# Optimization experiments

Hardware: AMD Instinct MI355X
Metric: run time of the kernel (lower is better)

Reference implementation:

```python
import jax, jax.numpy as jnp
import numpy as np
from jax import lax

N, CIN, COUT = 4, 3, 16
D = H = W = 64
K, S, PAD, OUT_PAD = 3, 2, 1, 1


def setup_inputs() -> dict:
    key = jax.random.key(0)
    k1, k2, k3, k4 = jax.random.split(key, 4)
    x = jax.random.normal(k1, (N, CIN, D, H, W), dtype=jnp.float32)
    # torch ConvTranspose3d weight layout: [Cin, Cout, kD, kH, kW]
    w = jax.random.normal(k2, (CIN, COUT, K, K, K), dtype=jnp.float32) * 0.1
    b = jax.random.normal(k3, (COUT,), dtype=jnp.float32) * 0.1
    subtract = jax.random.normal(k4, (COUT,), dtype=jnp.float32) * 0.1
    return {"x": x, "w": w, "b": b, "subtract": subtract}


def reference(x, w, b, subtract):
    # ConvTranspose3d(k=3, s=2, p=1, output_padding=1) as a dilated conv:
    # flip kernel spatially, swap in/out channel axes, lhs_dilation = stride,
    # padding low = k-1-p = 1, padding high = k-1-p+output_padding = 2.
    w_conv = jnp.flip(jnp.transpose(w, (1, 0, 2, 3, 4)), axis=(2, 3, 4))  # [Cout,Cin,k,k,k]
    y = lax.conv_general_dilated(
        x, w_conv,
        window_strides=(1, 1, 1),
        padding=[(1, 2), (1, 2), (1, 2)],
        lhs_dilation=(S, S, S),
        dimension_numbers=("NCDHW", "OIDHW", "NCDHW"),
    )  # [N, 16, 2D, 2H, 2W]
    y = y + b[None, :, None, None, None]
    # MaxPool3d(kernel=2, stride=2, pad=0)
    y = lax.reduce_window(
        y, -jnp.inf, lax.max,
        window_dimensions=(1, 1, 2, 2, 2),
        window_strides=(1, 1, 2, 2, 2),
        padding="VALID",
    )  # [N, 16, D, H, W]
    s = jax.nn.softmax(y, axis=1)                       # channel softmax
    z = s - subtract[None, :, None, None, None]          # per-channel subtract
    sw = z * jax.nn.sigmoid(z)                           # swish
    return jnp.max(sw, axis=1)                           # max over channels -> [N, D, H, W]
```

## Files before the change

kernel.cpp:

```cpp
#include <hip/hip_runtime.h>
#include <math.h>

#define CIN 3
#define COUT 16
#define DHW 64


typedef float f8 __attribute__((ext_vector_type(8)));
typedef float f2 __attribute__((ext_vector_type(2)));

struct WBuf { f8 a, b, c; f2 d2; float dl; };

template <int G>
static __device__ __forceinline__ void wload(WBuf& b, const char* wbase) {
    constexpr int J = G / 3, C = G % 3;
    constexpr int BOFF = (C * COUT + J) * 27 * 4;
    asm volatile(
        "s_load_dwordx8 %0, %5, %6\n\t"
        "s_load_dwordx8 %1, %5, %7\n\t"
        "s_load_dwordx8 %2, %5, %8\n\t"
        "s_load_dwordx2 %3, %5, %9\n\t"
        "s_load_dword   %4, %5, %10"
        : "=&s"(b.a), "=&s"(b.b), "=&s"(b.c), "=&s"(b.d2), "=&s"(b.dl)
        : "s"(wbase), "i"(BOFF), "i"(BOFF + 32), "i"(BOFF + 64),
          "i"(BOFF + 96), "i"(BOFF + 104));
}

static __device__ __forceinline__ void wwait(WBuf& b) {
    asm volatile("s_waitcnt lgkmcnt(0)"
                 : "+s"(b.a), "+s"(b.b), "+s"(b.c), "+s"(b.d2), "+s"(b.dl));
}

static __device__ __forceinline__ float welem(const WBuf& w, int k) {
    return k < 8 ? w.a[k] : k < 16 ? w.b[k - 8] : k < 24 ? w.c[k - 16]
                 : k < 26 ? w.d2[k - 24] : w.dl;
}

template <int C>
static __device__ __forceinline__ void fma_group(
    const WBuf& wb, const float (&xr)[CIN][3][2][3], float (&acc)[8][4]) {
#pragma unroll
    for (int kd = 0; kd < 3; ++kd) {
        const int pd  = (kd == 1) ? 0 : 1;
        const int dlt = (kd == 0) ? 1 : 0;
#pragma unroll
        for (int kh = 0; kh < 3; ++kh) {
            const int ph = (kh == 1) ? 0 : 1;
            const int hh = (kh == 0) ? 1 : 0;
#pragma unroll
            for (int kw = 0; kw < 3; ++kw) {
                const int pw = (kw == 1) ? 0 : 1;
                const int ww = (kw == 0) ? 1 : 0;
                const float wt = welem(wb, kd * 9 + kh * 3 + kw);
                const int q = (pd * 2 + ph) * 2 + pw;
#pragma unroll
                for (int dout = 0; dout < 2; ++dout)
#pragma unroll
                    for (int vx = 0; vx < 2; ++vx) {
                        const float xv = xr[C][dout + dlt][hh][ww + vx];
                        const int v = dout * 2 + vx;
                        if (C == 0 && kd < 2 && kh < 2 && kw < 2)
                            acc[q][v] = wt * xv;
                        else
                            acc[q][v] = fmaf(wt, xv, acc[q][v]);
                    }
            }
        }
    }
}

static __device__ __forceinline__ void pool_close(const float (&acc)[8][4],
                                                  float (&pc)[4]) {
#pragma unroll
    for (int v = 0; v < 4; ++v) {
        const float m01 = fmaxf(acc[0][v], acc[1][v]);
        const float m23 = fmaxf(acc[2][v], acc[3][v]);
        const float m45 = fmaxf(acc[4][v], acc[5][v]);
        const float m67 = fmaxf(acc[6][v], acc[7][v]);
        pc[v] = fmaxf(fmaxf(m01, m23), fmaxf(m45, m67));
    }
}

template <int G>
struct Pipe {
    static __device__ __forceinline__ void run(
        WBuf& A, WBuf& B, const char* wbase, const float (&xr)[CIN][3][2][3],
        float (&acc)[8][4], float (&pooled)[4][4]) {
        constexpr int J = G / 3, C = G % 3;
        WBuf& CUR = (G & 1) ? B : A;
        WBuf& NXT = (G & 1) ? A : B;
        wwait(CUR);
        __builtin_amdgcn_sched_barrier(0);
        if constexpr (G + 1 < 4 * CIN) wload<G + 1>(NXT, wbase);
        fma_group<C>(CUR, xr, acc);
        if constexpr (C == 2) pool_close(acc, pooled[J]);
        Pipe<G + 1>::run(A, B, wbase, xr, acc, pooled);
    }
};
template <>
struct Pipe<4 * CIN> {
    static __device__ __forceinline__ void run(
        WBuf&, WBuf&, const char*, const float (&)[CIN][3][2][3],
        float (&)[8][4], float (&)[4][4]) {}
};

__global__ __launch_bounds__(256) void fused_convt_pool_softmax_swish_max(
    const float* __restrict__ x,
    const float* __restrict__ w,
    const float* __restrict__ bias,
    const float* __restrict__ sub,
    float* __restrict__ out)
{
    __shared__ float xch[COUT][256];

    const int tid  = threadIdx.x;
    const int lane = tid & 63;
    const int wv   = __builtin_amdgcn_readfirstlane(tid >> 6);
    const int tp   = lane & 31;
    const int hr   = lane >> 5;
    const int hb   = blockIdx.x * 2;
    const int d0   = blockIdx.y * 2;
    const int n    = blockIdx.z;
    const int h    = hb + hr;
    const int w0   = tp * 2;

    float xr[CIN][3][2][3];
    const size_t nbase = (size_t)n * CIN * DHW * DHW * DHW;
    const bool w2ok = (w0 + 2 < DHW);
    const int  off2 = w2ok ? 2 : 0;
#pragma unroll
    for (int c = 0; c < CIN; ++c)
#pragma unroll
        for (int dd = 0; dd < 3; ++dd)
#pragma unroll
            for (int hh = 0; hh < 2; ++hh) {
                const int id = d0 + dd;
                const int ih = h + hh;
                float v0 = 0.0f, v1 = 0.0f, v2 = 0.0f;
                if (id < DHW && ih < DHW) {
                    const float* row =
                        x + nbase + (((size_t)c * DHW + id) * DHW + ih) * DHW + w0;
                    const float2 a = *(const float2*)row;
                    v0 = a.x;
                    v1 = a.y;
                    const float t = row[off2];
                    v2 = w2ok ? t : 0.0f;
                }
                asm volatile("" : "+v"(v0), "+v"(v1), "+v"(v2));
                xr[c][dd][hh][0] = v0;
                xr[c][dd][hh][1] = v1;
                xr[c][dd][hh][2] = v2;
            }

    const char* wbase = (const char*)w + (size_t)wv * 4 * 27 * 4;
    float pooled[4][4];
    float acc[8][4];
    WBuf A, B;
    wload<0>(A, wbase);
    Pipe<0>::run(A, B, wbase, xr, acc, pooled);

    const float* bj = (const float*)((const char*)bias + (size_t)wv * 16);
#pragma unroll
    for (int j = 0; j < 4; ++j) {
        const float b = bj[j];
        float4 v;
        v.x = pooled[j][0] + b;
        v.y = pooled[j][1] + b;
        v.z = pooled[j][2] + b;
        v.w = pooled[j][3] + b;
        *(float4*)&xch[wv * 4 + j][lane * 4] = v;
    }
    __syncthreads();

    float pv[COUT];
#pragma unroll
    for (int co = 0; co < COUT; ++co) pv[co] = xch[co][tid];
    float m = pv[0];
#pragma unroll
    for (int co = 1; co < COUT; ++co) m = fmaxf(m, pv[co]);
    float e[COUT];
    float s = 0.0f;
#pragma unroll
    for (int co = 0; co < COUT; ++co) {
        const float ev = __expf(pv[co] - m);
        e[co] = ev;
        s += ev;
    }
    const float inv = __builtin_amdgcn_rcpf(s);
    float zmax = -3.402823466e+38f;
#pragma unroll
    for (int co = 0; co < COUT; ++co)
        zmax = fmaxf(zmax, fmaf(e[co], inv, -sub[co]));
    const float res = zmax * __builtin_amdgcn_rcpf(1.0f + __expf(-zmax));

    const int vox  = tid & 3;
    const int sl   = tid >> 2;
    const int dout = vox >> 1;
    const int vx   = vox & 1;
    const int stp  = sl & 31;
    const int shr  = sl >> 5;
    out[(((size_t)n * DHW + (d0 + dout)) * DHW + (hb + shr)) * DHW + stp * 2 + vx] = res;
}

extern "C" void kernel_launch(void* const* d_in, const int* in_sizes, int n_in,
                              void* d_out, int out_size, void* d_ws, size_t ws_size,
                              hipStream_t stream) {
    const float* x   = (const float*)d_in[0];
    const float* w   = (const float*)d_in[1];
    const float* b   = (const float*)d_in[2];
    const float* sub = (const float*)d_in[3];
    float* out = (float*)d_out;

    dim3 block(256, 1, 1);
    dim3 grid(DHW / 2, DHW / 2, 4);
    fused_convt_pool_softmax_swish_max<<<grid, block, 0, stream>>>(x, w, b, sub, out);
}
```

Measured before the change: 118.2 us.

## Reload input patch per channel group instead of holding it in registers

The 54-float input patch is no longer held in registers for the whole kernel. Each pipeline step now reloads the 18 values for its input channel from global memory (cached), using precomputed clamped offsets and bitmasks in place of branches. A waves_per_eu(4,4) attribute is added to cap register use and target higher occupancy. The cost is four times more input loads, with latency that each FMA group may have to wait on.

```diff
diff --git a/kernel.cpp b/kernel.cpp
--- a/kernel.cpp
+++ b/kernel.cpp
@@ -36,9 +36,35 @@
                  : k < 26 ? w.d2[k - 24] : w.dl;
 }
 
+struct XBuf { float v[18]; };
+
+template <int C>
+static __device__ __forceinline__ void xload(
+    XBuf& xb, const char* xn, const int (&ro)[6], const int (&ro2)[6],
+    const unsigned (&mj)[6], const unsigned (&m2)[6]) {
+    const char* xc = xn + (size_t)C * (DHW * DHW * DHW * 4);
+#pragma unroll
+    for (int dd = 0; dd < 3; ++dd)
+#pragma unroll
+        for (int hh = 0; hh < 2; ++hh) {
+            const int r = dd * 2 + hh;
+            const float2 a = *(const float2*)(xc + ro[r]);
+            float v0 = a.x, v1 = a.y;
+            float t = *(const float*)(xc + ro2[r]);
+            if (dd == 2 || hh == 1) {
+                v0 = __uint_as_float(__float_as_uint(v0) & mj[r]);
+                v1 = __uint_as_float(__float_as_uint(v1) & mj[r]);
+            }
+            t = __uint_as_float(__float_as_uint(t) & m2[r]);
+            xb.v[r * 3 + 0] = v0;
+            xb.v[r * 3 + 1] = v1;
+            xb.v[r * 3 + 2] = t;
+        }
+}
+
 template <int C>
 static __device__ __forceinline__ void fma_group(
-    const WBuf& wb, const float (&xr)[CIN][3][2][3], float (&acc)[8][4]) {
+    const WBuf& wb, const XBuf& xb, float (&acc)[8][4]) {
 #pragma unroll
     for (int kd = 0; kd < 3; ++kd) {
         const int pd  = (kd == 1) ? 0 : 1;
@@ -57,7 +83,8 @@
                 for (int dout = 0; dout < 2; ++dout)
 #pragma unroll
                     for (int vx = 0; vx < 2; ++vx) {
-                        const float xv = xr[C][dout + dlt][hh][ww + vx];
+                        const float xv =
+                            xb.v[((dout + dlt) * 2 + hh) * 3 + (ww + vx)];
                         const int v = dout * 2 + vx;
                         if (C == 0 && kd < 2 && kh < 2 && kw < 2)
                             acc[q][v] = wt * xv;
@@ -84,27 +111,34 @@
 template <int G>
 struct Pipe {
     static __device__ __forceinline__ void run(
-        WBuf& A, WBuf& B, const char* wbase, const float (&xr)[CIN][3][2][3],
+        WBuf& A, WBuf& B, const char* wbase, const char* xn,
+        const int (&ro)[6], const int (&ro2)[6],
+        const unsigned (&mj)[6], const unsigned (&m2)[6],
         float (&acc)[8][4], float (&pooled)[4][4]) {
         constexpr int J = G / 3, C = G % 3;
         WBuf& CUR = (G & 1) ? B : A;
         WBuf& NXT = (G & 1) ? A : B;
         wwait(CUR);
         __builtin_amdgcn_sched_barrier(0);
+        XBuf xb;
+        xload<C>(xb, xn, ro, ro2, mj, m2);
         if constexpr (G + 1 < 4 * CIN) wload<G + 1>(NXT, wbase);
-        fma_group<C>(CUR, xr, acc);
+        fma_group<C>(CUR, xb, acc);
         if constexpr (C == 2) pool_close(acc, pooled[J]);
-        Pipe<G + 1>::run(A, B, wbase, xr, acc, pooled);
+        Pipe<G + 1>::run(A, B, wbase, xn, ro, ro2, mj, m2, acc, pooled);
     }
 };
 template <>
 struct Pipe<4 * CIN> {
     static __device__ __forceinline__ void run(
-        WBuf&, WBuf&, const char*, const float (&)[CIN][3][2][3],
+        WBuf&, WBuf&, const char*, const char*, const int (&)[6],
+        const int (&)[6], const unsigned (&)[6], const unsigned (&)[6],
         float (&)[8][4], float (&)[4][4]) {}
 };
 
-__global__ __launch_bounds__(256) void fused_convt_pool_softmax_swish_max(
+__global__ __launch_bounds__(256)
+__attribute__((amdgpu_waves_per_eu(4, 4)))
+void fused_convt_pool_softmax_swish_max(
     const float* __restrict__ x,
     const float* __restrict__ w,
     const float* __restrict__ bias,
@@ -124,40 +158,32 @@
     const int h    = hb + hr;
     const int w0   = tp * 2;
 
-    float xr[CIN][3][2][3];
-    const size_t nbase = (size_t)n * CIN * DHW * DHW * DHW;
+    const char* xn = (const char*)x + (size_t)n * CIN * DHW * DHW * DHW * 4;
     const bool w2ok = (w0 + 2 < DHW);
-    const int  off2 = w2ok ? 2 : 0;
-#pragma unroll
-    for (int c = 0; c < CIN; ++c)
-#pragma unroll
-        for (int dd = 0; dd < 3; ++dd)
-#pragma unroll
-            for (int hh = 0; hh < 2; ++hh) {
-                const int id = d0 + dd;
-                const int ih = h + hh;
-                float v0 = 0.0f, v1 = 0.0f, v2 = 0.0f;
-                if (id < DHW && ih < DHW) {
-                    const float* row =
-                        x + nbase + (((size_t)c * DHW + id) * DHW + ih) * DHW + w0;
-                    const float2 a = *(const float2*)row;
-                    v0 = a.x;
-                    v1 = a.y;
-                    const float t = row[off2];
-                    v2 = w2ok ? t : 0.0f;
-                }
-                asm volatile("" : "+v"(v0), "+v"(v1), "+v"(v2));
-                xr[c][dd][hh][0] = v0;
-                xr[c][dd][hh][1] = v1;
-                xr[c][dd][hh][2] = v2;
-            }
+    const unsigned wm = w2ok ? ~0u : 0u;
+    const int d2 = w2ok ? 8 : 4;
+    int ro[6], ro2[6];
+    unsigned mj[6], m2[6];
+#pragma unroll
+    for (int dd = 0; dd < 3; ++dd)
+#pragma unroll
+        for (int hh = 0; hh < 2; ++hh) {
+            const int r  = dd * 2 + hh;
+            const int id = min(d0 + dd, DHW - 1);
+            const int ih = min(h + hh, DHW - 1);
+            ro[r]  = ((id * DHW + ih) * DHW + w0) * 4;
+            ro2[r] = ro[r] + d2;
+            const bool ok = (d0 + dd < DHW) && (h + hh < DHW);
+            mj[r] = ok ? ~0u : 0u;
+            m2[r] = mj[r] & wm;
+        }
 
     const char* wbase = (const char*)w + (size_t)wv * 4 * 27 * 4;
     float pooled[4][4];
     float acc[8][4];
     WBuf A, B;
     wload<0>(A, wbase);
-    Pipe<0>::run(A, B, wbase, xr, acc, pooled);
+    Pipe<0>::run(A, B, wbase, xn, ro, ro2, mj, m2, acc, pooled);
 
     const float* bj = (const float*)((const char*)bias + (size_t)wv * 16);
 #pragma unroll
```

After: 139.1 us. 1.18x slower.
